# Kernel optimization log

Measured on AMD Instinct MI355X. Metric: run time of the kernel, lower is better.

The kernel has to match this reference:

```python
import jax, jax.numpy as jnp
import numpy as np

B, D, H, DH = 2048, 1024, 8, 64  # batch, query_dim, heads, dim_head
INNER = H * DH  # 512


def setup_inputs() -> dict:
    key = jax.random.key(0)
    k0, k1, k2, k3 = jax.random.split(key, 4)
    x = jax.random.normal(k0, (B, D), dtype=jnp.float32)
    Wq = jax.random.normal(k1, (D, INNER), dtype=jnp.float32) * 0.02
    Wkv = jax.random.normal(k2, (D, 2 * INNER), dtype=jnp.float32) * 0.02
    Wout = jax.random.normal(k3, (INNER, D), dtype=jnp.float32) * 0.02
    bout = jnp.zeros((D,), dtype=jnp.float32)
    return {"x": x, "Wq": Wq, "Wkv": Wkv, "Wout": Wout, "bout": bout}


def reference(x, Wq, Wkv, Wout, bout):
    # Faithful to the original: 2D x, attention over the flattened (B*H) axis.
    b = x.shape[0]
    scale = DH ** -0.5
    q = (x @ Wq).reshape(b * H, DH)            # (b h) d
    k, v = jnp.split(x @ Wkv, 2, axis=-1)      # each [b, inner]
    k = k.reshape(b * H, DH)
    v = v.reshape(b * H, DH)
    sim = (q @ k.T) * scale                    # [(b h), (b h)] -- 1 GB intermediate
    attn = jax.nn.softmax(sim, axis=-1)        # dropout_rate = 0 -> identity
    out = (attn @ v).reshape(b, INNER)         # b (h d)
    return out @ Wout + bout                   # project_out path
```

## Files before the change

### kernel.cpp

```cpp
#include <hip/hip_runtime.h>
#include <hip/hip_bf16.h>
#include <stdint.h>


typedef __bf16 bf16_t;
typedef __bf16 bf16x4 __attribute__((ext_vector_type(4)));
typedef __bf16 bf16x8 __attribute__((ext_vector_type(8)));
typedef float floatx4 __attribute__((ext_vector_type(4)));

__device__ __forceinline__ floatx4 mfma16(bf16x8 a, bf16x8 b, floatx4 c) {
    return __builtin_amdgcn_mfma_f32_16x16x32_bf16(a, b, c, 0, 0, 0);
}

__device__ __forceinline__ bf16x8 cvt8(float4 a, float4 b) {
    bf16x8 o;
    o[0] = (bf16_t)a.x; o[1] = (bf16_t)a.y; o[2] = (bf16_t)a.z; o[3] = (bf16_t)a.w;
    o[4] = (bf16_t)b.x; o[5] = (bf16_t)b.y; o[6] = (bf16_t)b.z; o[7] = (bf16_t)b.w;
    return o;
}

__device__ __forceinline__ void transpose_body(const float* __restrict__ in, int N,
                                               bf16_t* __restrict__ out, int ldo,
                                               int bx, int by, int tid, float (*tile)[33]) {
    int n0 = bx * 32, k0 = by * 32;
    int tx = tid & 31, ty = tid >> 5;
#pragma unroll
    for (int i = 0; i < 32; i += 8)
        tile[ty + i][tx] = in[(size_t)(k0 + ty + i) * N + (n0 + tx)];
    __syncthreads();
#pragma unroll
    for (int i = 0; i < 32; i += 8)
        out[(size_t)(n0 + ty + i) * ldo + (k0 + tx)] = (bf16_t)tile[tx][ty + i];
}

__global__ __launch_bounds__(256) void prep_all(const float* __restrict__ x,
                                                bf16_t* __restrict__ xb,
                                                const float* __restrict__ Wq,
                                                const float* __restrict__ Wkv,
                                                const float* __restrict__ Wout,
                                                bf16_t* __restrict__ WtQKV,
                                                bf16_t* __restrict__ WtOut) {
    __shared__ float tile[32][33];
    int b = blockIdx.x, tid = threadIdx.x;
    if (b < 1024) {
        int i = (b * 256 + tid) * 8;
        *(bf16x8*)(xb + i) = cvt8(*(const float4*)(x + i), *(const float4*)(x + i + 4));
    } else if (b < 1536) {
        b -= 1024;
        transpose_body(Wq, 512, WtQKV, 1024, b & 15, b >> 4, tid, tile);
    } else if (b < 2560) {
        b -= 1536;
        transpose_body(Wkv, 1024, WtQKV + 512 * 1024, 1024, b & 31, b >> 5, tid, tile);
    } else {
        b -= 2560;
        transpose_body(Wout, 1024, WtOut, 512, b & 31, b >> 5, tid, tile);
    }
}

template <int OF32, int MI>
__global__ __launch_bounds__(256) void gemm_bt(const bf16_t* __restrict__ A,
                                               const bf16_t* __restrict__ Bt,
                                               const float* __restrict__ bias,
                                               void* __restrict__ Cout,
                                               bf16_t* __restrict__ VtOut, int vt_col0,
                                               int K, int lda, int ldb, int ldc,
                                               float qscale, int qcols) {
    constexpr int MT = MI * 32;
    constexpr int PA = MT / 64;
    __shared__ bf16_t sA[MT * 64];
    __shared__ bf16_t sB[64 * 64];
    int tid = threadIdx.x;
    int wave = tid >> 6, lane = tid & 63;
    int lm = lane & 15, q = lane >> 4;
    int bm = blockIdx.x * MT, bn = blockIdx.y * 64;
    int wm = (wave >> 1) * (MT / 2), wn = (wave & 1) * 32;

    int c0 = (tid & 3) * 2, c1 = c0 + 1;
    int rA[PA], swA[PA];
    size_t srcA0[PA], srcA1[PA];
#pragma unroll
    for (int p = 0; p < PA; ++p) {
        rA[p] = p * 64 + (tid >> 2);
        swA[p] = rA[p] & 7;
        srcA0[p] = (size_t)(bm + rA[p]) * lda + ((c0 ^ swA[p]) << 3);
        srcA1[p] = (size_t)(bm + rA[p]) * lda + ((c1 ^ swA[p]) << 3);
    }
    int rB = tid >> 2, swB = rB & 7;
    size_t srcB0 = (size_t)(bn + rB) * ldb + ((c0 ^ swB) << 3);
    size_t srcB1 = (size_t)(bn + rB) * ldb + ((c1 ^ swB) << 3);

    floatx4 acc[MI][2];
#pragma unroll
    for (int i = 0; i < MI; ++i)
#pragma unroll
        for (int j = 0; j < 2; ++j) acc[i][j] = (floatx4){0.f, 0.f, 0.f, 0.f};

    bf16x8 pa0[PA], pa1[PA], pb0, pb1;
#pragma unroll
    for (int p = 0; p < PA; ++p) {
        pa0[p] = *(const bf16x8*)(A + srcA0[p]);
        pa1[p] = *(const bf16x8*)(A + srcA1[p]);
    }
    pb0 = *(const bf16x8*)(Bt + srcB0);
    pb1 = *(const bf16x8*)(Bt + srcB1);
#pragma unroll
    for (int p = 0; p < PA; ++p) {
        *(bf16x8*)&sA[p * 4096 + tid * 16] = pa0[p];
        *(bf16x8*)&sA[p * 4096 + tid * 16 + 8] = pa1[p];
    }
    *(bf16x8*)&sB[tid * 16] = pb0;
    *(bf16x8*)&sB[tid * 16 + 8] = pb1;
    __syncthreads();

    for (int k0 = 0; k0 < K; k0 += 64) {
        int kn = (k0 + 64 < K) ? k0 + 64 : 0;
#pragma unroll
        for (int p = 0; p < PA; ++p) {
            pa0[p] = *(const bf16x8*)(A + srcA0[p] + kn);
            pa1[p] = *(const bf16x8*)(A + srcA1[p] + kn);
        }
        pb0 = *(const bf16x8*)(Bt + srcB0 + kn);
        pb1 = *(const bf16x8*)(Bt + srcB1 + kn);

#pragma unroll
        for (int s = 0; s < 2; ++s) {
            int cs = s * 4 + q;
            bf16x8 af[MI], bfr[2];
#pragma unroll
            for (int i = 0; i < MI; ++i) {
                int row = wm + i * 16 + lm;
                af[i] = *(bf16x8*)&sA[row * 64 + ((cs ^ (lm & 7)) << 3)];
            }
#pragma unroll
            for (int j = 0; j < 2; ++j) {
                int row = wn + j * 16 + lm;
                bfr[j] = *(bf16x8*)&sB[row * 64 + ((cs ^ (lm & 7)) << 3)];
            }
#pragma unroll
            for (int i = 0; i < MI; ++i)
#pragma unroll
                for (int j = 0; j < 2; ++j)
                    acc[i][j] = mfma16(af[i], bfr[j], acc[i][j]);
        }

        __syncthreads();
#pragma unroll
        for (int p = 0; p < PA; ++p) {
            *(bf16x8*)&sA[p * 4096 + tid * 16] = pa0[p];
            *(bf16x8*)&sA[p * 4096 + tid * 16 + 8] = pa1[p];
        }
        *(bf16x8*)&sB[tid * 16] = pb0;
        *(bf16x8*)&sB[tid * 16 + 8] = pb1;
        __syncthreads();
    }

#pragma unroll
    for (int i = 0; i < MI; ++i)
#pragma unroll
        for (int j = 0; j < 2; ++j)
#pragma unroll
            for (int r = 0; r < 4; ++r) {
                int row = bm + wm + i * 16 + q * 4 + r;
                int col = bn + wn + j * 16 + lm;
                float v = acc[i][j][r];
                if (col < qcols) v *= qscale;
                if (bias) v += bias[col];
                if (col >= vt_col0) {
                    int cc = col - vt_col0;
                    VtOut[(size_t)(cc & 63) * 16384 + row * 8 + (cc >> 6)] = (bf16_t)v;
                } else {
                    size_t off = (size_t)row * ldc + col;
                    if (OF32) ((float*)Cout)[off] = v;
                    else      ((bf16_t*)Cout)[off] = (bf16_t)v;
                }
            }
}

__global__ __launch_bounds__(256, 2) void flash_attn(const bf16_t* __restrict__ QK,
                                                     const bf16_t* __restrict__ Vt,
                                                     bf16_t* __restrict__ O,
                                                     float* __restrict__ accP,
                                                     float* __restrict__ lP,
                                                     int kps, int nsplit) {
    __shared__ bf16_t sK[64 * 64];
    __shared__ bf16_t sVt[64 * 64];
    int tid = threadIdx.x;
    int wave = tid >> 6, lane = tid & 63;
    int lm = lane & 15, q = lane >> 4;
    int sp = blockIdx.y;
    int qrow0 = blockIdx.x * 256 + wave * 64;

    bf16x8 qf[4][2];
#pragma unroll
    for (int sub = 0; sub < 4; ++sub) {
        int qr = qrow0 + sub * 16 + lm;
        const bf16_t* qp = QK + (size_t)(qr >> 3) * 1024 + (qr & 7) * 64;
        qf[sub][0] = *(const bf16x8*)(qp + q * 8);
        qf[sub][1] = *(const bf16x8*)(qp + 32 + q * 8);
    }

    int sr = tid >> 2;
    int ch0 = (tid & 3) * 2, ch1 = ch0 + 1;
    int swz = sr & 7;
    int lsr = 32 * (sr >> 5) + 8 * ((sr >> 2) & 3) + 4 * ((sr >> 4) & 1) + (sr & 3);
    int ksrcA = (lsr >> 3) * 1024 + (lsr & 7) * 64 + 512 + ((ch0 ^ swz) << 3);
    int ksrcB = (lsr >> 3) * 1024 + (lsr & 7) * 64 + 512 + ((ch1 ^ swz) << 3);
    size_t vsrcA = (size_t)sr * 16384 + ((ch0 ^ swz) << 3);
    size_t vsrcB = (size_t)sr * 16384 + ((ch1 ^ swz) << 3);
    bf16_t* dK = &sK[tid * 16];
    bf16_t* dV = &sVt[tid * 16];

    int c0 = q ^ (lm & 7);

    floatx4 acc[4][4];
#pragma unroll
    for (int sub = 0; sub < 4; ++sub)
#pragma unroll
        for (int i = 0; i < 4; ++i) acc[sub][i] = (floatx4){0.f, 0.f, 0.f, 0.f};
    float lacc[4] = {0.f, 0.f, 0.f, 0.f};

    int kt0 = sp * kps, kend = kt0 + kps;

    bf16x8 krA, krB, vrA, vrB;
    {
        const bf16_t* kb = QK + (size_t)kt0 * 128;
        krA = *(const bf16x8*)(kb + ksrcA);
        krB = *(const bf16x8*)(kb + ksrcB);
        vrA = *(const bf16x8*)(Vt + vsrcA + kt0);
        vrB = *(const bf16x8*)(Vt + vsrcB + kt0);
    }
    *(bf16x8*)dK = krA; *(bf16x8*)(dK + 8) = krB;
    *(bf16x8*)dV = vrA; *(bf16x8*)(dV + 8) = vrB;
    __syncthreads();

    for (int kt = kt0; kt < kend; kt += 64) {
        int ktn = (kt + 64 < kend) ? kt + 64 : kt0;
        const bf16_t* kbn = QK + (size_t)ktn * 128;
        krA = *(const bf16x8*)(kbn + ksrcA);
        krB = *(const bf16x8*)(kbn + ksrcB);
        vrA = *(const bf16x8*)(Vt + vsrcA + ktn);
        vrB = *(const bf16x8*)(Vt + vsrcB + ktn);

        floatx4 s[4][4];
#pragma unroll
        for (int nb = 0; nb < 4; ++nb) {
            int row = (nb * 16 + lm) * 64;
            bf16x8 k0 = *(bf16x8*)&sK[row + (c0 << 3)];
            bf16x8 k1 = *(bf16x8*)&sK[row + ((c0 ^ 4) << 3)];
#pragma unroll
            for (int sub = 0; sub < 4; ++sub) {
                floatx4 a = (floatx4){0.f, 0.f, 0.f, 0.f};
                a = mfma16(k0, qf[sub][0], a);
                a = mfma16(k1, qf[sub][1], a);
                s[sub][nb] = a;
            }
        }

        bf16x8 pf[4][2];
#pragma unroll
        for (int sub = 0; sub < 4; ++sub) {
#pragma unroll
            for (int nb = 0; nb < 4; ++nb)
#pragma unroll
                for (int r = 0; r < 4; ++r) {
                    float pv = __builtin_amdgcn_exp2f(s[sub][nb][r]);
                    s[sub][nb][r] = pv;
                    lacc[sub] += pv;
                }
#pragma unroll
            for (int jb = 0; jb < 2; ++jb) {
                bf16x8 p;
#pragma unroll
                for (int r = 0; r < 4; ++r) {
                    p[r] = (bf16_t)s[sub][2 * jb][r];
                    p[r + 4] = (bf16_t)s[sub][2 * jb + 1][r];
                }
                pf[sub][jb] = p;
            }
        }

#pragma unroll
        for (int jb = 0; jb < 2; ++jb) {
            bf16x8 av[4];
#pragma unroll
            for (int nd = 0; nd < 4; ++nd)
                av[nd] = *(bf16x8*)&sVt[(nd * 16 + lm) * 64 + ((c0 ^ (jb << 2)) << 3)];
#pragma unroll
            for (int sub = 0; sub < 4; ++sub)
#pragma unroll
                for (int nd = 0; nd < 4; ++nd)
                    acc[sub][nd] = mfma16(av[nd], pf[sub][jb], acc[sub][nd]);
        }

        __syncthreads();
        *(bf16x8*)dK = krA; *(bf16x8*)(dK + 8) = krB;
        *(bf16x8*)dV = vrA; *(bf16x8*)(dV + 8) = vrB;
        __syncthreads();
    }

#pragma unroll
    for (int sub = 0; sub < 4; ++sub) {
        lacc[sub] += __shfl_xor(lacc[sub], 16);
        lacc[sub] += __shfl_xor(lacc[sub], 32);
    }

    if (nsplit == 1) {
#pragma unroll
        for (int sub = 0; sub < 4; ++sub) {
            float inv = 1.f / lacc[sub];
            int row = qrow0 + sub * 16 + lm;
#pragma unroll
            for (int nd = 0; nd < 4; ++nd) {
                bf16x4 o;
#pragma unroll
                for (int r = 0; r < 4; ++r) o[r] = (bf16_t)(acc[sub][nd][r] * inv);
                *(bf16x4*)&O[(size_t)row * 64 + nd * 16 + q * 4] = o;
            }
        }
    } else {
#pragma unroll
        for (int sub = 0; sub < 4; ++sub) {
            int row = qrow0 + sub * 16 + lm;
            size_t base = ((size_t)sp * 16384 + row) * 64;
#pragma unroll
            for (int nd = 0; nd < 4; ++nd) {
                float4 v = {acc[sub][nd][0], acc[sub][nd][1],
                            acc[sub][nd][2], acc[sub][nd][3]};
                *(float4*)&accP[base + nd * 16 + q * 4] = v;
            }
            if (lane < 16) lP[sp * 16384 + row] = lacc[sub];
        }
    }
}

__global__ __launch_bounds__(256) void merge_attn(const float* __restrict__ accP,
                                                  const float* __restrict__ lP,
                                                  bf16_t* __restrict__ O, int nsplit) {
    int idx = blockIdx.x * 256 + threadIdx.x;
    int row = idx >> 4, dh4 = (idx & 15) * 4;
    float4 num = {0.f, 0.f, 0.f, 0.f};
    float den = 0.f;
    for (int s = 0; s < nsplit; ++s) {
        float4 a = *(const float4*)&accP[((size_t)s * 16384 + row) * 64 + dh4];
        num.x += a.x; num.y += a.y; num.z += a.z; num.w += a.w;
        den += lP[s * 16384 + row];
    }
    float inv = 1.f / den;
    bf16x4 o;
    o[0] = (bf16_t)(num.x * inv); o[1] = (bf16_t)(num.y * inv);
    o[2] = (bf16_t)(num.z * inv); o[3] = (bf16_t)(num.w * inv);
    *(bf16x4*)&O[(size_t)row * 64 + dh4] = o;
}

extern "C" void kernel_launch(void* const* d_in, const int* in_sizes, int n_in,
                              void* d_out, int out_size, void* d_ws, size_t ws_size,
                              hipStream_t stream) {
    const float* x    = (const float*)d_in[0];
    const float* Wq   = (const float*)d_in[1];
    const float* Wkv  = (const float*)d_in[2];
    const float* Wout = (const float*)d_in[3];
    const float* bout = (const float*)d_in[4];

    char* ws = (char*)d_ws;
    bf16_t* QK    = (bf16_t*)ws;
    bf16_t* Vt    = (bf16_t*)(ws + 4194304);
    bf16_t* Ob    = (bf16_t*)(ws + 6291456);
    bf16_t* xb    = (bf16_t*)(ws + 8388608);
    bf16_t* WtQKV = (bf16_t*)(ws + 12582912);
    bf16_t* WtOut = (bf16_t*)(ws + 15728640);
    float*  accP  = (float*)(ws + 16777216);

    int nsplit = (ws_size >= (size_t)16777216 + 8 * 4259840) ? 8
               : (ws_size >= (size_t)16777216 + 4 * 4259840) ? 4
               : (ws_size >= (size_t)16777216 + 2 * 4259840) ? 2 : 1;
    float* lP = (float*)(ws + 16777216 + (size_t)nsplit * 4194304);

    prep_all<<<3072, 256, 0, stream>>>(x, xb, Wq, Wkv, Wout, WtQKV, WtOut);

    gemm_bt<0, 2><<<dim3(32, 24), 256, 0, stream>>>(
        xb, WtQKV, nullptr, QK, Vt, 1024, 1024, 1024, 1024, 1024,
        0.18033688011112042f, 512);

    flash_attn<<<dim3(64, nsplit), 256, 0, stream>>>(QK, Vt, Ob, accP, lP,
                                                     16384 / nsplit, nsplit);
    if (nsplit > 1)
        merge_attn<<<1024, 256, 0, stream>>>(accP, lP, Ob, nsplit);

    gemm_bt<1, 2><<<dim3(32, 16), 256, 0, stream>>>(
        Ob, WtOut, bout, d_out, nullptr, 1 << 30, 512, 512, 512, 1024,
        1.0f, 0);
}
```

Measured before the change: 172.8 us.

## Double-buffer K/V shared tiles and raise wave priority around MFMA phases

```diff
diff --git a/kernel.cpp b/kernel.cpp
--- a/kernel.cpp
+++ b/kernel.cpp
@@ -182,8 +182,8 @@
                                                      float* __restrict__ accP,
                                                      float* __restrict__ lP,
                                                      int kps, int nsplit) {
-    __shared__ bf16_t sK[64 * 64];
-    __shared__ bf16_t sVt[64 * 64];
+    __shared__ bf16_t sK[2][64 * 64];
+    __shared__ bf16_t sVt[2][64 * 64];
     int tid = threadIdx.x;
     int wave = tid >> 6, lane = tid & 63;
     int lm = lane & 15, q = lane >> 4;
@@ -207,8 +207,6 @@
     int ksrcB = (lsr >> 3) * 1024 + (lsr & 7) * 64 + 512 + ((ch1 ^ swz) << 3);
     size_t vsrcA = (size_t)sr * 16384 + ((ch0 ^ swz) << 3);
     size_t vsrcB = (size_t)sr * 16384 + ((ch1 ^ swz) << 3);
-    bf16_t* dK = &sK[tid * 16];
-    bf16_t* dV = &sVt[tid * 16];
 
     int c0 = q ^ (lm & 7);
 
@@ -229,10 +227,11 @@
         vrA = *(const bf16x8*)(Vt + vsrcA + kt0);
         vrB = *(const bf16x8*)(Vt + vsrcB + kt0);
     }
-    *(bf16x8*)dK = krA; *(bf16x8*)(dK + 8) = krB;
-    *(bf16x8*)dV = vrA; *(bf16x8*)(dV + 8) = vrB;
+    *(bf16x8*)&sK[0][tid * 16] = krA; *(bf16x8*)&sK[0][tid * 16 + 8] = krB;
+    *(bf16x8*)&sVt[0][tid * 16] = vrA; *(bf16x8*)&sVt[0][tid * 16 + 8] = vrB;
     __syncthreads();
 
+    int cur = 0;
     for (int kt = kt0; kt < kend; kt += 64) {
         int ktn = (kt + 64 < kend) ? kt + 64 : kt0;
         const bf16_t* kbn = QK + (size_t)ktn * 128;
@@ -241,12 +240,16 @@
         vrA = *(const bf16x8*)(Vt + vsrcA + ktn);
         vrB = *(const bf16x8*)(Vt + vsrcB + ktn);
 
+        const bf16_t* cK = sK[cur];
+        const bf16_t* cV = sVt[cur];
+
         floatx4 s[4][4];
+        __builtin_amdgcn_s_setprio(1);
 #pragma unroll
         for (int nb = 0; nb < 4; ++nb) {
             int row = (nb * 16 + lm) * 64;
-            bf16x8 k0 = *(bf16x8*)&sK[row + (c0 << 3)];
-            bf16x8 k1 = *(bf16x8*)&sK[row + ((c0 ^ 4) << 3)];
+            bf16x8 k0 = *(const bf16x8*)&cK[row + (c0 << 3)];
+            bf16x8 k1 = *(const bf16x8*)&cK[row + ((c0 ^ 4) << 3)];
 #pragma unroll
             for (int sub = 0; sub < 4; ++sub) {
                 floatx4 a = (floatx4){0.f, 0.f, 0.f, 0.f};
@@ -255,6 +258,7 @@
                 s[sub][nb] = a;
             }
         }
+        __builtin_amdgcn_s_setprio(0);
 
         bf16x8 pf[4][2];
 #pragma unroll
@@ -279,23 +283,27 @@
             }
         }
 
+        __builtin_amdgcn_s_setprio(1);
 #pragma unroll
         for (int jb = 0; jb < 2; ++jb) {
             bf16x8 av[4];
 #pragma unroll
             for (int nd = 0; nd < 4; ++nd)
-                av[nd] = *(bf16x8*)&sVt[(nd * 16 + lm) * 64 + ((c0 ^ (jb << 2)) << 3)];
+                av[nd] = *(const bf16x8*)&cV[(nd * 16 + lm) * 64 + ((c0 ^ (jb << 2)) << 3)];
 #pragma unroll
             for (int sub = 0; sub < 4; ++sub)
 #pragma unroll
                 for (int nd = 0; nd < 4; ++nd)
                     acc[sub][nd] = mfma16(av[nd], pf[sub][jb], acc[sub][nd]);
         }
-
+        __builtin_amdgcn_s_setprio(0);
+
+        bf16_t* nK = &sK[cur ^ 1][tid * 16];
+        bf16_t* nV = &sVt[cur ^ 1][tid * 16];
+        *(bf16x8*)nK = krA; *(bf16x8*)(nK + 8) = krB;
+        *(bf16x8*)nV = vrA; *(bf16x8*)(nV + 8) = vrB;
         __syncthreads();
-        *(bf16x8*)dK = krA; *(bf16x8*)(dK + 8) = krB;
-        *(bf16x8*)dV = vrA; *(bf16x8*)(dV + 8) = vrB;
-        __syncthreads();
+        cur ^= 1;
     }
 
 #pragma unroll
```

Result: no change. 172.4 us (-0.3%).

## Load K and V fragments directly from global into registers, drop LDS staging

Applied to the files above, without the earlier changes.

```diff
diff --git a/kernel.cpp b/kernel.cpp
--- a/kernel.cpp
+++ b/kernel.cpp
@@ -182,8 +182,6 @@
                                                      float* __restrict__ accP,
                                                      float* __restrict__ lP,
                                                      int kps, int nsplit) {
-    __shared__ bf16_t sK[64 * 64];
-    __shared__ bf16_t sVt[64 * 64];
     int tid = threadIdx.x;
     int wave = tid >> 6, lane = tid & 63;
     int lm = lane & 15, q = lane >> 4;
@@ -199,18 +197,16 @@
         qf[sub][1] = *(const bf16x8*)(qp + 32 + q * 8);
     }
 
-    int sr = tid >> 2;
-    int ch0 = (tid & 3) * 2, ch1 = ch0 + 1;
-    int swz = sr & 7;
-    int lsr = 32 * (sr >> 5) + 8 * ((sr >> 2) & 3) + 4 * ((sr >> 4) & 1) + (sr & 3);
-    int ksrcA = (lsr >> 3) * 1024 + (lsr & 7) * 64 + 512 + ((ch0 ^ swz) << 3);
-    int ksrcB = (lsr >> 3) * 1024 + (lsr & 7) * 64 + 512 + ((ch1 ^ swz) << 3);
-    size_t vsrcA = (size_t)sr * 16384 + ((ch0 ^ swz) << 3);
-    size_t vsrcB = (size_t)sr * 16384 + ((ch1 ^ swz) << 3);
-    bf16_t* dK = &sK[tid * 16];
-    bf16_t* dV = &sVt[tid * 16];
-
-    int c0 = q ^ (lm & 7);
+    int koff[4];
+#pragma unroll
+    for (int nb = 0; nb < 4; ++nb) {
+        int lk = 32 * (nb >> 1) + 8 * (lm >> 2) + 4 * (nb & 1) + (lm & 3);
+        koff[nb] = (lk >> 3) * 1024 + (lk & 7) * 64 + 512 + q * 8;
+    }
+    size_t voff[4];
+#pragma unroll
+    for (int nd = 0; nd < 4; ++nd)
+        voff[nd] = (size_t)(nd * 16 + lm) * 16384 + q * 8;
 
     floatx4 acc[4][4];
 #pragma unroll
@@ -221,82 +217,84 @@
 
     int kt0 = sp * kps, kend = kt0 + kps;
 
-    bf16x8 krA, krB, vrA, vrB;
+    bf16x8 kA[4][2], kB[4][2];
     {
         const bf16_t* kb = QK + (size_t)kt0 * 128;
-        krA = *(const bf16x8*)(kb + ksrcA);
-        krB = *(const bf16x8*)(kb + ksrcB);
-        vrA = *(const bf16x8*)(Vt + vsrcA + kt0);
-        vrB = *(const bf16x8*)(Vt + vsrcB + kt0);
-    }
-    *(bf16x8*)dK = krA; *(bf16x8*)(dK + 8) = krB;
-    *(bf16x8*)dV = vrA; *(bf16x8*)(dV + 8) = vrB;
-    __syncthreads();
-
-    for (int kt = kt0; kt < kend; kt += 64) {
-        int ktn = (kt + 64 < kend) ? kt + 64 : kt0;
-        const bf16_t* kbn = QK + (size_t)ktn * 128;
-        krA = *(const bf16x8*)(kbn + ksrcA);
-        krB = *(const bf16x8*)(kbn + ksrcB);
-        vrA = *(const bf16x8*)(Vt + vsrcA + ktn);
-        vrB = *(const bf16x8*)(Vt + vsrcB + ktn);
-
-        floatx4 s[4][4];
 #pragma unroll
         for (int nb = 0; nb < 4; ++nb) {
-            int row = (nb * 16 + lm) * 64;
-            bf16x8 k0 = *(bf16x8*)&sK[row + (c0 << 3)];
-            bf16x8 k1 = *(bf16x8*)&sK[row + ((c0 ^ 4) << 3)];
-#pragma unroll
-            for (int sub = 0; sub < 4; ++sub) {
-                floatx4 a = (floatx4){0.f, 0.f, 0.f, 0.f};
-                a = mfma16(k0, qf[sub][0], a);
-                a = mfma16(k1, qf[sub][1], a);
-                s[sub][nb] = a;
-            }
-        }
-
-        bf16x8 pf[4][2];
-#pragma unroll
-        for (int sub = 0; sub < 4; ++sub) {
-#pragma unroll
-            for (int nb = 0; nb < 4; ++nb)
-#pragma unroll
-                for (int r = 0; r < 4; ++r) {
-                    float pv = __builtin_amdgcn_exp2f(s[sub][nb][r]);
-                    s[sub][nb][r] = pv;
-                    lacc[sub] += pv;
-                }
-#pragma unroll
-            for (int jb = 0; jb < 2; ++jb) {
-                bf16x8 p;
-#pragma unroll
-                for (int r = 0; r < 4; ++r) {
-                    p[r] = (bf16_t)s[sub][2 * jb][r];
-                    p[r + 4] = (bf16_t)s[sub][2 * jb + 1][r];
-                }
-                pf[sub][jb] = p;
-            }
-        }
-
-#pragma unroll
-        for (int jb = 0; jb < 2; ++jb) {
-            bf16x8 av[4];
-#pragma unroll
-            for (int nd = 0; nd < 4; ++nd)
-                av[nd] = *(bf16x8*)&sVt[(nd * 16 + lm) * 64 + ((c0 ^ (jb << 2)) << 3)];
-#pragma unroll
-            for (int sub = 0; sub < 4; ++sub)
-#pragma unroll
-                for (int nd = 0; nd < 4; ++nd)
-                    acc[sub][nd] = mfma16(av[nd], pf[sub][jb], acc[sub][nd]);
-        }
-
-        __syncthreads();
-        *(bf16x8*)dK = krA; *(bf16x8*)(dK + 8) = krB;
-        *(bf16x8*)dV = vrA; *(bf16x8*)(dV + 8) = vrB;
-        __syncthreads();
-    }
+            kA[nb][0] = *(const bf16x8*)(kb + koff[nb]);
+            kA[nb][1] = *(const bf16x8*)(kb + koff[nb] + 32);
+        }
+    }
+
+#define ATTN_TILE(KC, KN, KT_V, KT_N)                                              \
+    {                                                                              \
+        bf16x8 vf[4][2];                                                           \
+        const bf16_t* vb_ = Vt + (KT_V);                                           \
+        _Pragma("unroll")                                                          \
+        for (int nd = 0; nd < 4; ++nd) {                                           \
+            vf[nd][0] = *(const bf16x8*)(vb_ + voff[nd]);                          \
+            vf[nd][1] = *(const bf16x8*)(vb_ + voff[nd] + 32);                     \
+        }                                                                          \
+        const bf16_t* kbn_ = QK + (size_t)(KT_N) * 128;                            \
+        _Pragma("unroll")                                                          \
+        for (int nb = 0; nb < 4; ++nb) {                                           \
+            KN[nb][0] = *(const bf16x8*)(kbn_ + koff[nb]);                         \
+            KN[nb][1] = *(const bf16x8*)(kbn_ + koff[nb] + 32);                    \
+        }                                                                          \
+        floatx4 s_[4][4];                                                          \
+        __builtin_amdgcn_s_setprio(1);                                             \
+        _Pragma("unroll")                                                          \
+        for (int nb = 0; nb < 4; ++nb) {                                           \
+            _Pragma("unroll")                                                      \
+            for (int sub = 0; sub < 4; ++sub) {                                    \
+                floatx4 a_ = (floatx4){0.f, 0.f, 0.f, 0.f};                        \
+                a_ = mfma16(KC[nb][0], qf[sub][0], a_);                            \
+                a_ = mfma16(KC[nb][1], qf[sub][1], a_);                            \
+                s_[sub][nb] = a_;                                                  \
+            }                                                                      \
+        }                                                                          \
+        __builtin_amdgcn_s_setprio(0);                                             \
+        bf16x8 pf[4][2];                                                           \
+        _Pragma("unroll")                                                          \
+        for (int sub = 0; sub < 4; ++sub) {                                        \
+            _Pragma("unroll")                                                      \
+            for (int nb = 0; nb < 4; ++nb) {                                       \
+                _Pragma("unroll")                                                  \
+                for (int r = 0; r < 4; ++r) {                                      \
+                    float pv_ = __builtin_amdgcn_exp2f(s_[sub][nb][r]);            \
+                    s_[sub][nb][r] = pv_;                                          \
+                    lacc[sub] += pv_;                                              \
+                }                                                                  \
+            }                                                                      \
+            _Pragma("unroll")                                                      \
+            for (int jb = 0; jb < 2; ++jb) {                                       \
+                bf16x8 p_;                                                         \
+                _Pragma("unroll")                                                  \
+                for (int r = 0; r < 4; ++r) {                                      \
+                    p_[r] = (bf16_t)s_[sub][2 * jb][r];                            \
+                    p_[r + 4] = (bf16_t)s_[sub][2 * jb + 1][r];                    \
+                }                                                                  \
+                pf[sub][jb] = p_;                                                  \
+            }                                                                      \
+        }                                                                          \
+        __builtin_amdgcn_s_setprio(1);                                             \
+        _Pragma("unroll")                                                          \
+        for (int jb = 0; jb < 2; ++jb)                                             \
+            _Pragma("unroll")                                                      \
+            for (int sub = 0; sub < 4; ++sub)                                      \
+                _Pragma("unroll")                                                  \
+                for (int nd = 0; nd < 4; ++nd)                                     \
+                    acc[sub][nd] = mfma16(vf[nd][jb], pf[sub][jb], acc[sub][nd]);  \
+        __builtin_amdgcn_s_setprio(0);                                             \
+    }
+
+    for (int kt = kt0; kt < kend; kt += 128) {
+        int ktn2 = (kt + 128 < kend) ? kt + 128 : kt0;
+        ATTN_TILE(kA, kB, kt, kt + 64);
+        ATTN_TILE(kB, kA, kt + 64, ktn2);
+    }
+#undef ATTN_TILE
 
 #pragma unroll
     for (int sub = 0; sub < 4; ++sub) {
```

Result: slower. 364.9 us (+111.1%).
